# Kernel optimization log

Measured on AMD Instinct MI355X. Metric: run time of the kernel, lower is better.

## Reference

```python
import jax, jax.numpy as jnp
import numpy as np
import math

H, D = 8, 128            # num_heads, head_dim (hidden=1024)
CHUNK, PAST, FUT = 12, 12, 0
CTX = CHUNK + PAST + FUT  # 24
SOFTCAP = 50.0
INVALID = 1e-09
Q_SCALE = D ** (-0.5) / math.log(2)
K_SCALE = math.log(1.0 + math.e) / math.log(2)


def setup_inputs() -> dict:
    key = jax.random.key(0)
    ks = jax.random.split(key, 7)
    B, S, HS = 16, 2400, 1024
    w = lambda k: jax.random.normal(k, (HS, HS), jnp.float32) * 0.02
    return {
        "x": jax.random.normal(ks[0], (B, S, HS), jnp.float32),
        "pos_emb": jax.random.normal(ks[1], (CTX + 1, HS), jnp.float32),
        "Wq": w(ks[2]),
        "Wk": w(ks[3]),
        "Wv": w(ks[4]),
        "Wpost": w(ks[5]),
        "Wrel": w(ks[6]),
        "per_dim_scale": jnp.zeros((D,), jnp.float32),
    }


def _to_blocks(t):
    # [B,S,H,D] -> [B,nb,CHUNK,H,D] (pad S up to multiple of CHUNK)
    B, S, h, d = t.shape
    nb = -(-S // CHUNK)
    t = jnp.pad(t, ((0, 0), (0, nb * CHUNK - S), (0, 0), (0, 0)))
    return t.reshape(B, nb, CHUNK, h, d)


def _block_context(t):
    # [B,S,H,D] -> [B,nb,CTX,H,D]: per-block window of PAST left context + chunk + FUT
    B, S, h, d = t.shape
    nb = -(-S // CHUNK)
    tp = jnp.pad(t, ((0, 0), (PAST, FUT + CHUNK - 1), (0, 0), (0, 0)))
    idx = jnp.arange(nb)[:, None] * CHUNK + jnp.arange(CTX)[None, :]  # [nb,CTX]
    return tp[:, idx]  # gather -> [B,nb,CTX,H,D]


def _rel_shift(x):
    # [B,H,nb,CHUNK,P] -> [B,H,nb,CHUNK,CTX] via Transformer-XL reshape trick
    B, h, nb, bs, P = x.shape
    x = jnp.pad(x, ((0, 0), (0, 0), (0, 0), (0, 0), (0, CTX + 1 - P)))
    x = x.reshape(B, h, nb, bs * (CTX + 1))[..., : bs * CTX]
    return x.reshape(B, h, nb, bs, CTX)


def reference(x, pos_emb, Wq, Wk, Wv, Wpost, Wrel, per_dim_scale):
    B, S, HS = x.shape
    q = (x @ Wq).reshape(B, S, H, D) * Q_SCALE * jax.nn.softplus(per_dim_scale)
    k = (x @ Wk).reshape(B, S, H, D) * K_SCALE
    v = (x @ Wv).reshape(B, S, H, D)

    qb = _to_blocks(q)        # [B,nb,CHUNK,H,D]
    kc = _block_context(k)    # [B,nb,CTX,H,D]
    vc = _block_context(v)    # [B,nb,CTX,H,D]
    nb = qb.shape[1]

    rel_k = (pos_emb @ Wrel).reshape(-1, H, D)  # [P,H,D]

    # content-content scores: [B,H,nb,CHUNK,CTX]
    matrix_ac = jnp.einsum('bnqhd,bnkhd->bhnqk', qb, kc)
    # content-position scores with rel-shift: [B,H,nb,CHUNK,P] -> [...,CTX]
    matrix_bd = jnp.einsum('bnqhd,phd->bhnqp', qb, rel_k)
    matrix_bd = _rel_shift(matrix_bd)

    attn = jnp.tanh((matrix_ac + matrix_bd) / SOFTCAP) * SOFTCAP
    attn = jax.nn.softmax(attn, axis=-1)

    out = jnp.einsum('bhnqk,bnkhd->bnqhd', attn, vc)  # [B,nb,CHUNK,H,D]
    out = out.reshape(B, nb * CHUNK, H * D)[:, :S, :]
    return out @ Wpost
```

## Files before the change

### kernel.cpp

```cpp
#include <hip/hip_runtime.h>
#include <hip/hip_bf16.h>
#include <cmath>

#define AS_GLOBAL __attribute__((address_space(1)))
#define AS_LDS    __attribute__((address_space(3)))

typedef __attribute__((ext_vector_type(8))) short bf16x8;
typedef __attribute__((ext_vector_type(4))) float f32x4;
typedef unsigned short u16;

__device__ __forceinline__ u16 f2bf(float f) {
  union { __hip_bfloat16 h; u16 u; } cv;
  cv.h = __float2bfloat16(f);
  return cv.u;
}
__device__ __forceinline__ float bf2f(u16 u) {
  union { unsigned u32; float f; } v;
  v.u32 = ((unsigned)u) << 16;
  return v.f;
}


__global__ void k_f32_to_bf16(const float* __restrict__ in, u16* __restrict__ out, int n4) {
  int i = blockIdx.x * 256 + threadIdx.x;
  if (i >= n4) return;
  float4 v = ((const float4*)in)[i];
  ushort4 o;
  o.x = f2bf(v.x); o.y = f2bf(v.y); o.z = f2bf(v.z); o.w = f2bf(v.w);
  ((ushort4*)out)[i] = o;
}

__global__ void k_transpose_w(const float* __restrict__ in, u16* __restrict__ out) {
  __shared__ float tile[32][33];
  const int tx = threadIdx.x & 31;
  const int ty = threadIdx.x >> 5;
  const int x0 = blockIdx.x * 32, y0 = blockIdx.y * 32;
  #pragma unroll
  for (int i = 0; i < 32; i += 8)
    tile[ty + i][tx] = in[(size_t)(y0 + ty + i) * 1024 + x0 + tx];
  __syncthreads();
  #pragma unroll
  for (int i = 0; i < 32; i += 8)
    out[(size_t)(x0 + ty + i) * 1024 + y0 + tx] = f2bf(tile[tx][ty + i]);
}

__global__ void k_qscale(const float* __restrict__ pds, float* __restrict__ qs, float qscale_c) {
  int n = blockIdx.x * 256 + threadIdx.x;
  float s = pds[n & 127];
  qs[n] = qscale_c * log1pf(expf(s));
}

__global__ void k_relk(const float* __restrict__ pos, const u16* __restrict__ wrt,
                       u16* __restrict__ relkb) {
  __shared__ float prow[1024];
  const int tid = threadIdx.x;
  const int p = blockIdx.y;
  ((float4*)prow)[tid] = ((const float4*)(pos + (size_t)p * 1024))[tid];
  __syncthreads();
  int nn = blockIdx.x * 256 + tid;
  const u16* wr = wrt + (size_t)nn * 1024;
  float acc = 0.f;
  for (int kk = 0; kk < 1024; kk += 8) {
    ushort4 u0 = *(const ushort4*)(wr + kk);
    ushort4 u1 = *(const ushort4*)(wr + kk + 4);
    acc += bf2f(u0.x) * prow[kk + 0] + bf2f(u0.y) * prow[kk + 1]
         + bf2f(u0.z) * prow[kk + 2] + bf2f(u0.w) * prow[kk + 3]
         + bf2f(u1.x) * prow[kk + 4] + bf2f(u1.y) * prow[kk + 5]
         + bf2f(u1.z) * prow[kk + 6] + bf2f(u1.w) * prow[kk + 7];
  }
  relkb[(size_t)p * 1024 + nn] = f2bf(acc);
}

template <int OUTMODE>
__global__ __launch_bounds__(256) void k_gemm_bt(
    const u16* __restrict__ A, const u16* __restrict__ Bt, void* __restrict__ Cout,
    const float* __restrict__ scale_vec, float scale_scalar, int M, int N, int K) {
  __shared__ __align__(16) u16 As[128 * 32];
  __shared__ __align__(16) u16 Bs[128 * 32];
  const int tid = threadIdx.x;
  const int wave = tid >> 6, lane = tid & 63;
  const int quad = lane >> 4, l16 = lane & 15;
  const int wm = wave >> 1, wn = wave & 1;
  const int m0 = blockIdx.y * 128, n0 = blockIdx.x * 128;

  f32x4 acc[4][4];
  #pragma unroll
  for (int i = 0; i < 4; ++i)
    #pragma unroll
    for (int j = 0; j < 4; ++j) {
      f32x4 z = {0.f, 0.f, 0.f, 0.f};
      acc[i][j] = z;
    }

  for (int k0 = 0; k0 < K; k0 += 32) {
    __syncthreads();
    #pragma unroll
    for (int i = 0; i < 2; ++i) {
      int cbase = i * 256 + wave * 64;
      int c = cbase + lane;
      const u16* ga = A + (size_t)(m0 + (c >> 2)) * K + (k0 + (c & 3) * 8);
      __builtin_amdgcn_global_load_lds((const AS_GLOBAL u16*)ga, (AS_LDS u16*)&As[cbase * 8], 16, 0, 0);
      const u16* gb = Bt + (size_t)(n0 + (c >> 2)) * K + (k0 + (c & 3) * 8);
      __builtin_amdgcn_global_load_lds((const AS_GLOBAL u16*)gb, (AS_LDS u16*)&Bs[cbase * 8], 16, 0, 0);
    }
    __syncthreads();

    bf16x8 af[4], bfr[4];
    #pragma unroll
    for (int mi = 0; mi < 4; ++mi)
      af[mi] = *(const bf16x8*)&As[(wm * 64 + mi * 16 + l16) * 32 + quad * 8];
    #pragma unroll
    for (int ni = 0; ni < 4; ++ni)
      bfr[ni] = *(const bf16x8*)&Bs[(wn * 64 + ni * 16 + l16) * 32 + quad * 8];
    #pragma unroll
    for (int mi = 0; mi < 4; ++mi)
      #pragma unroll
      for (int ni = 0; ni < 4; ++ni)
        acc[mi][ni] = __builtin_amdgcn_mfma_f32_16x16x32_bf16(af[mi], bfr[ni], acc[mi][ni], 0, 0, 0);
  }

  if (OUTMODE == 2) {
    #pragma unroll
    for (int ni = 0; ni < 4; ++ni) {
      int col = n0 + wn * 64 + ni * 16 + l16;
      #pragma unroll
      for (int mi = 0; mi < 4; ++mi) {
        int row = m0 + wm * 64 + mi * 16 + quad * 4;
        ushort4 o;
        o.x = f2bf(acc[mi][ni][0]);
        o.y = f2bf(acc[mi][ni][1]);
        o.z = f2bf(acc[mi][ni][2]);
        o.w = f2bf(acc[mi][ni][3]);
        *(ushort4*)&((u16*)Cout)[(size_t)col * M + row] = o;
      }
    }
  } else {
    #pragma unroll
    for (int ni = 0; ni < 4; ++ni) {
      int col = n0 + wn * 64 + ni * 16 + l16;
      float cs = scale_vec ? scale_vec[col] : scale_scalar;
      #pragma unroll
      for (int mi = 0; mi < 4; ++mi) {
        int row = m0 + wm * 64 + mi * 16 + quad * 4;
        #pragma unroll
        for (int r = 0; r < 4; ++r) {
          float v = acc[mi][ni][r] * cs;
          if (OUTMODE == 1)
            ((u16*)Cout)[(size_t)(row + r) * N + col] = f2bf(v);
          else
            ((float*)Cout)[(size_t)(row + r) * N + col] = v;
        }
      }
    }
  }
}

__global__ __launch_bounds__(256) void k_attn_mfma(
    const u16* __restrict__ q, const u16* __restrict__ k, const u16* __restrict__ vt,
    const u16* __restrict__ relkb, u16* __restrict__ ctx) {
  __shared__ float bdm_s[4][400];
  __shared__ u16 attnb[4][16 * 32];

  const int tid = threadIdx.x;
  const int w = tid >> 6, lane = tid & 63;
  const int l16 = lane & 15, quad = lane >> 4;
  const int id = blockIdx.x * 4 + w;
  const int b = id / 1600;
  const int rr = id % 1600;
  const int n = rr >> 3, h = rr & 7;
  const int s0 = n * 12;
  const size_t rowbase = (size_t)b * 2400;

  bf16x8 qf[4];
  {
    int sq = s0 + l16;
    if (sq > 2399) sq = 2399;
    const u16* qp = q + ((rowbase + sq) * 1024 + (size_t)h * 128 + quad * 8);
    #pragma unroll
    for (int c = 0; c < 4; ++c) qf[c] = *(const bf16x8*)(qp + 32 * c);
  }

  #pragma unroll
  for (int pt = 0; pt < 2; ++pt) {
    int p = pt * 16 + l16;
    const u16* rp = relkb + ((size_t)p * 1024 + (size_t)h * 128 + quad * 8);
    f32x4 acc = {0.f, 0.f, 0.f, 0.f};
    #pragma unroll
    for (int c = 0; c < 4; ++c)
      acc = __builtin_amdgcn_mfma_f32_16x16x32_bf16(qf[c], *(const bf16x8*)(rp + 32 * c), acc, 0, 0, 0);
    if (p < 25) {
      #pragma unroll
      for (int r = 0; r < 4; ++r)
        bdm_s[w][(quad * 4 + r) * 25 + p] = acc[r];
    }
  }
  __threadfence_block();

  float l0[4], l1[4];
  #pragma unroll
  for (int kt = 0; kt < 2; ++kt) {
    int t = kt * 16 + l16;
    int sk = s0 - 12 + t;
    bool kvalid = ((unsigned)sk < 2400u);
    int ska = kvalid ? sk : 0;
    const u16* kp = k + ((rowbase + ska) * 1024 + (size_t)h * 128 + quad * 8);
    short km = kvalid ? (short)0xFFFF : (short)0;
    bf16x8 kmv = {km, km, km, km, km, km, km, km};
    f32x4 acc = {0.f, 0.f, 0.f, 0.f};
    #pragma unroll
    for (int c = 0; c < 4; ++c) {
      bf16x8 kf = *(const bf16x8*)(kp + 32 * c);
      kf &= kmv;
      acc = __builtin_amdgcn_mfma_f32_16x16x32_bf16(qf[c], kf, acc, 0, 0, 0);
    }
    #pragma unroll
    for (int r = 0; r < 4; ++r) {
      float bd = bdm_s[w][(quad * 4 + r) * 24 + t];
      float lg = tanhf((acc[r] + bd) * (1.0f / 50.0f)) * 50.0f;
      if (kt == 1 && l16 >= 8) lg = -INFINITY;
      if (kt) l1[r] = lg; else l0[r] = lg;
    }
  }

  float at0[4], at1[4];
  #pragma unroll
  for (int r = 0; r < 4; ++r) {
    float m = fmaxf(l0[r], l1[r]);
    #pragma unroll
    for (int s = 1; s < 16; s <<= 1) m = fmaxf(m, __shfl_xor(m, s, 64));
    float e0 = __expf(l0[r] - m), e1 = __expf(l1[r] - m);
    float sum = e0 + e1;
    #pragma unroll
    for (int s = 1; s < 16; s <<= 1) sum += __shfl_xor(sum, s, 64);
    float inv = 1.0f / sum;
    at0[r] = e0 * inv;
    at1[r] = e1 * inv;
  }

  #pragma unroll
  for (int r = 0; r < 4; ++r) {
    attnb[w][(quad * 4 + r) * 32 + l16] = f2bf(at0[r]);
    attnb[w][(quad * 4 + r) * 32 + 16 + l16] = f2bf(at1[r]);
  }
  __threadfence_block();
  bf16x8 af = *(const bf16x8*)&attnb[w][l16 * 32 + quad * 8];

  int slo = s0 - 12 + quad * 8;
  bf16x8 vmsk;
  #pragma unroll
  for (int j = 0; j < 8; ++j)
    vmsk[j] = ((unsigned)(slo + j) < 2400u) ? (short)0xFFFF : (short)0;

  f32x4 oacc[8];
  #pragma unroll
  for (int dt = 0; dt < 8; ++dt) {
    int col = h * 128 + dt * 16 + l16;
    const u16* vp = vt + ((size_t)col * 38400 + (long)(rowbase + s0 - 12 + quad * 8));
    ushort4 va = *(const ushort4*)vp;
    ushort4 vb = *(const ushort4*)(vp + 4);
    bf16x8 vf = {(short)va.x, (short)va.y, (short)va.z, (short)va.w,
                 (short)vb.x, (short)vb.y, (short)vb.z, (short)vb.w};
    vf &= vmsk;
    f32x4 z = {0.f, 0.f, 0.f, 0.f};
    oacc[dt] = __builtin_amdgcn_mfma_f32_16x16x32_bf16(af, vf, z, 0, 0, 0);
  }

  if (quad < 3) {
    #pragma unroll
    for (int dt = 0; dt < 8; ++dt) {
      int col = h * 128 + dt * 16 + l16;
      #pragma unroll
      for (int r = 0; r < 4; ++r) {
        int qi = quad * 4 + r;
        ctx[(rowbase + s0 + qi) * 1024 + col] = f2bf(oacc[dt][r]);
      }
    }
  }
}


extern "C" void kernel_launch(void* const* d_in, const int* in_sizes, int n_in,
                              void* d_out, int out_size, void* d_ws, size_t ws_size,
                              hipStream_t stream) {
  const float* x       = (const float*)d_in[0];
  const float* pos_emb = (const float*)d_in[1];
  const float* Wq      = (const float*)d_in[2];
  const float* Wk      = (const float*)d_in[3];
  const float* Wv      = (const float*)d_in[4];
  const float* Wpost   = (const float*)d_in[5];
  const float* Wrel    = (const float*)d_in[6];
  const float* pds     = (const float*)d_in[7];
  float* out = (float*)d_out;

  const int M = 38400, HS = 1024;
  const size_t XE = (size_t)M * HS;

  u16* xbf = (u16*)d_ws;
  u16* qbf = xbf + XE;
  u16* kbf = qbf + XE;
  u16* vt_alloc = kbf + XE;
  u16* vt = vt_alloc + 16;
  u16* wqt = vt_alloc + XE + 64;
  u16* wkt = wqt + (size_t)HS * HS;
  u16* wvt = wkt + (size_t)HS * HS;
  u16* wrt = wvt + (size_t)HS * HS;
  u16* wpt = wrt + (size_t)HS * HS;
  u16* relkb = wpt + (size_t)HS * HS;
  float* qsc = (float*)(relkb + 32 * 1024);

  const double LN2 = 0.6931471805599453;
  const float QS = (float)((1.0 / sqrt(128.0)) / LN2);
  const float KS = (float)(log(1.0 + exp(1.0)) / LN2);

  k_f32_to_bf16<<<(int)(XE / 4 / 256), 256, 0, stream>>>(x, xbf, (int)(XE / 4));
  dim3 tg(32, 32);
  k_transpose_w<<<tg, 256, 0, stream>>>(Wq, wqt);
  k_transpose_w<<<tg, 256, 0, stream>>>(Wk, wkt);
  k_transpose_w<<<tg, 256, 0, stream>>>(Wv, wvt);
  k_transpose_w<<<tg, 256, 0, stream>>>(Wrel, wrt);
  k_transpose_w<<<tg, 256, 0, stream>>>(Wpost, wpt);
  k_qscale<<<4, 256, 0, stream>>>(pds, qsc, QS);
  k_relk<<<dim3(4, 25), 256, 0, stream>>>(pos_emb, wrt, relkb);
  dim3 gg(HS / 128, M / 128);
  k_gemm_bt<1><<<gg, 256, 0, stream>>>(xbf, wqt, qbf, qsc, 1.0f, M, HS, HS);
  k_gemm_bt<1><<<gg, 256, 0, stream>>>(xbf, wkt, kbf, nullptr, KS, M, HS, HS);
  k_gemm_bt<2><<<gg, 256, 0, stream>>>(xbf, wvt, vt, nullptr, 1.0f, M, HS, HS);
  k_attn_mfma<<<25600 / 4, 256, 0, stream>>>(qbf, kbf, vt, relkb, xbf);
  k_gemm_bt<0><<<gg, 256, 0, stream>>>(xbf, wpt, out, nullptr, 1.0f, M, HS, HS);
}
```

Before: 950.4 us.

## Replace GEMMs with pipelined 256x256 tile kernel, fuse QKV, persistent attention

Replaces the simple 128x128 GEMM with a 256x256-tile, 512-thread kernel. The new kernel double-buffers LDS through direct global-to-LDS loads, uses swizzled LDS addressing, interleaves MFMA with fine-grained waitcnt/barrier staging, and applies a grid-swizzled tile order. The Q, K and V projections become one launch over a concatenated N=3072 weight, with section-specific epilogues. The attention kernel becomes a grid-stride loop over 2048 blocks. The intent is higher MFMA utilisation and fewer launches, at the cost of relying on wqt/wkt/wvt being contiguous and on K being a multiple of 128.

```diff
diff --git a/kernel.cpp b/kernel.cpp
--- a/kernel.cpp
+++ b/kernel.cpp
@@ -71,89 +71,203 @@
   relkb[(size_t)p * 1024 + nn] = f2bf(acc);
 }
 
-template <int OUTMODE>
-__global__ __launch_bounds__(256) void k_gemm_bt(
-    const u16* __restrict__ A, const u16* __restrict__ Bt, void* __restrict__ Cout,
-    const float* __restrict__ scale_vec, float scale_scalar, int M, int N, int K) {
-  __shared__ __align__(16) u16 As[128 * 32];
-  __shared__ __align__(16) u16 Bs[128 * 32];
-  const int tid = threadIdx.x;
-  const int wave = tid >> 6, lane = tid & 63;
-  const int quad = lane >> 4, l16 = lane & 15;
-  const int wm = wave >> 1, wn = wave & 1;
-  const int m0 = blockIdx.y * 128, n0 = blockIdx.x * 128;
-
-  f32x4 acc[4][4];
+
+#define VMCNT(n) do { asm volatile("s_waitcnt vmcnt(" #n ")" ::: "memory"); \
+                      __builtin_amdgcn_sched_barrier(0); } while (0)
+#define BARF() do { asm volatile("" ::: "memory"); __builtin_amdgcn_s_barrier(); asm volatile("" ::: "memory"); } while (0)
+#define GLD(SRC, DST) __builtin_amdgcn_global_load_lds((const AS_GLOBAL u16*)(SRC), (AS_LDS u16*)(DST), 16, 0, 0)
+#define LDSA(d) ((AS_LDS char*)&lds[d][0][0])
+#define LDSB(d) ((AS_LDS char*)&lds[d][1][0])
+
+#define STAGE_A(d, h, t) do {                                                   \
+  GLD(sA0 + (((size_t)(h)) << 6) * K + ((t) << 6), LDSA(d) + dA0 + ((h) << 13)); \
+  GLD(sA1 + (((size_t)(h)) << 6) * K + ((t) << 6), LDSA(d) + dA1 + ((h) << 13)); \
+} while (0)
+#define STAGE_B(d, h, t) do {                                                   \
+  GLD(sB0 + (((size_t)(h)) << 5) * K + ((t) << 6), LDSB(d) + dB0 + ((h) << 12)); \
+  GLD(sB1 + (((size_t)(h)) << 5) * K + ((t) << 6), LDSB(d) + dB1 + ((h) << 12)); \
+} while (0)
+
+#define LOAD_A(d, qm) do {                                                       \
+  _Pragma("unroll") for (int mi_ = 0; mi_ < 4; ++mi_) {                          \
+    af[mi_][0] = *(const bf16x8*)&lds[d][0][abase + (((qm)*64 + mi_*16) << 6) + gk0]; \
+    af[mi_][1] = *(const bf16x8*)&lds[d][0][abase + (((qm)*64 + mi_*16) << 6) + gk1]; \
+  } } while (0)
+#define LOAD_B(d, qn) do {                                                       \
+  _Pragma("unroll") for (int ni_ = 0; ni_ < 2; ++ni_) {                          \
+    bfb[ni_][0] = *(const bf16x8*)&lds[d][1][bbase + (((qn)*32 + ni_*16) << 6) + gk0]; \
+    bfb[ni_][1] = *(const bf16x8*)&lds[d][1][bbase + (((qn)*32 + ni_*16) << 6) + gk1]; \
+  } } while (0)
+#define MFMA16(qm, qn) do {                                                      \
+  __builtin_amdgcn_s_setprio(1);                                                 \
+  _Pragma("unroll") for (int mi_ = 0; mi_ < 4; ++mi_)                            \
+  _Pragma("unroll") for (int ni_ = 0; ni_ < 2; ++ni_) {                          \
+    acc[(qm)*4+mi_][(qn)*2+ni_] = __builtin_amdgcn_mfma_f32_16x16x32_bf16(       \
+        af[mi_][0], bfb[ni_][0], acc[(qm)*4+mi_][(qn)*2+ni_], 0, 0, 0);          \
+    acc[(qm)*4+mi_][(qn)*2+ni_] = __builtin_amdgcn_mfma_f32_16x16x32_bf16(       \
+        af[mi_][1], bfb[ni_][1], acc[(qm)*4+mi_][(qn)*2+ni_], 0, 0, 0);          \
+  }                                                                              \
+  __builtin_amdgcn_s_setprio(0); } while (0)
+
+#define GEMM_MAINLOOP()                                                          \
+  STAGE_B(0, 0, 0);  STAGE_A(0, 1, 0);  STAGE_A(0, 0, 0);  STAGE_B(0, 1, 0);     \
+  STAGE_B(1, 0, 1);  STAGE_A(1, 1, 1);                                           \
+  VMCNT(6);  BARF();                                                             \
+  const int nk = K >> 6;                                                         \
+  for (int i = 0; i < (nk >> 1) - 1; ++i) {                                      \
+    const int t1 = 2 * i + 1, t2 = 2 * i + 2, t3 = 2 * i + 3;                    \
+    LOAD_A(0, 0); LOAD_B(0, 0);                                                  \
+    STAGE_A(1, 0, t1);                                                           \
+    BARF(); MFMA16(0, 0); BARF();                                                \
+    LOAD_A(0, 1);                                                                \
+    STAGE_B(1, 1, t1);                                                           \
+    BARF(); MFMA16(1, 0); VMCNT(8); BARF();                                      \
+    LOAD_B(0, 1);                                                                \
+    STAGE_B(0, 0, t2);                                                           \
+    BARF(); MFMA16(1, 1); BARF();                                                \
+    LOAD_A(0, 0);                                                                \
+    STAGE_A(0, 1, t2);                                                           \
+    BARF(); MFMA16(0, 1); VMCNT(6); BARF();                                      \
+    LOAD_A(1, 0); LOAD_B(1, 0);                                                  \
+    STAGE_A(0, 0, t2);                                                           \
+    BARF(); MFMA16(0, 0); BARF();                                                \
+    LOAD_A(1, 1);                                                                \
+    STAGE_B(0, 1, t2);                                                           \
+    BARF(); MFMA16(1, 0); VMCNT(8); BARF();                                      \
+    LOAD_B(1, 1);                                                                \
+    STAGE_B(1, 0, t3);                                                           \
+    BARF(); MFMA16(1, 1); BARF();                                                \
+    LOAD_A(1, 0);                                                                \
+    STAGE_A(1, 1, t3);                                                           \
+    BARF(); MFMA16(0, 1); VMCNT(6); BARF();                                      \
+  }                                                                              \
+  {                                                                              \
+    const int t1 = nk - 1;                                                       \
+    LOAD_A(0, 0); LOAD_B(0, 0);                                                  \
+    STAGE_A(1, 0, t1);                                                           \
+    BARF(); MFMA16(0, 0); BARF();                                                \
+    LOAD_A(0, 1);                                                                \
+    STAGE_B(1, 1, t1);                                                           \
+    BARF(); MFMA16(1, 0); VMCNT(8); BARF();                                      \
+    LOAD_B(0, 1);                                                                \
+    BARF(); MFMA16(1, 1); BARF();                                                \
+    LOAD_A(0, 0);                                                                \
+    BARF(); MFMA16(0, 1); VMCNT(2); BARF();                                      \
+    LOAD_A(1, 0); LOAD_B(1, 0);                                                  \
+    BARF(); MFMA16(0, 0); BARF();                                                \
+    LOAD_A(1, 1);                                                                \
+    BARF(); MFMA16(1, 0); VMCNT(0); BARF();                                      \
+    LOAD_B(1, 1);                                                                \
+    BARF(); MFMA16(1, 1); BARF();                                                \
+    LOAD_A(1, 0);                                                                \
+    BARF(); MFMA16(0, 1);                                                        \
+  }
+
+#define GEMM_SETUP(NTN)                                                          \
+  __shared__ __align__(16) u16 lds[2][2][16384];                                 \
+  const int tid = threadIdx.x;                                                   \
+  const int wave = tid >> 6, lane = tid & 63;                                    \
+  const int l16 = lane & 15, quad = lane >> 4;                                   \
+  const int wm = wave >> 2, wn = wave & 3;                                       \
+  const int q8 = (int)gridDim.x >> 3;                                            \
+  const int wg = ((int)blockIdx.x & 7) * q8 + ((int)blockIdx.x >> 3);            \
+  const int m0 = (wg / (NTN)) << 8;                                              \
+  const int n0 = (wg % (NTN)) << 8;                                              \
+  const int sx = l16 & 7;                                                        \
+  const int gk0 = (quad ^ sx) << 3;                                              \
+  const int gk1 = ((4 + quad) ^ sx) << 3;                                        \
+  const int abase = (wm * 128 + l16) << 6;                                       \
+  const int bbase = (wn * 64 + l16) << 6;                                        \
+  const int rl0 = tid >> 3, g0 = tid & 7;                                        \
+  const int rl1 = rl0 + 64;                                                      \
+  const int swz0 = (g0 ^ (rl0 & 7)) << 3;                                        \
+  const int rbA0 = ((rl0 >> 6) << 7) + (rl0 & 63);                               \
+  const int rbA1 = ((rl1 >> 6) << 7) + (rl1 & 63);                               \
+  const int rbB0 = ((rl0 >> 5) << 6) + (rl0 & 31);                               \
+  const int rbB1 = ((rl1 >> 5) << 6) + (rl1 & 31);                               \
+  const u16* sA0 = A + (size_t)(m0 + rbA0) * K + swz0;                           \
+  const u16* sA1 = A + (size_t)(m0 + rbA1) * K + swz0;                           \
+  const u16* sB0 = Bt + (size_t)(n0 + rbB0) * K + swz0;                          \
+  const u16* sB1 = Bt + (size_t)(n0 + rbB1) * K + swz0;                          \
+  const int dA0 = (rbA0 << 7) + (g0 << 4);                                       \
+  const int dA1 = (rbA1 << 7) + (g0 << 4);                                       \
+  const int dB0 = (rbB0 << 7) + (g0 << 4);                                       \
+  const int dB1 = (rbB1 << 7) + (g0 << 4);                                       \
+  f32x4 acc[8][4];                                                               \
+  _Pragma("unroll") for (int i = 0; i < 8; ++i)                                  \
+    _Pragma("unroll") for (int j = 0; j < 4; ++j) {                              \
+      f32x4 z = {0.f, 0.f, 0.f, 0.f};                                            \
+      acc[i][j] = z;                                                             \
+    }                                                                            \
+  bf16x8 af[4][2], bfb[2][2];
+
+__global__ __launch_bounds__(512, 2) void k_gemm256(
+    const u16* __restrict__ A, const u16* __restrict__ Bt, float* __restrict__ Cout,
+    int M, int N, int K) {
+  GEMM_SETUP(N >> 8)
+  GEMM_MAINLOOP()
+  const int mb = m0 + wm * 128, nb = n0 + wn * 64;
   #pragma unroll
-  for (int i = 0; i < 4; ++i)
-    #pragma unroll
-    for (int j = 0; j < 4; ++j) {
-      f32x4 z = {0.f, 0.f, 0.f, 0.f};
-      acc[i][j] = z;
-    }
-
-  for (int k0 = 0; k0 < K; k0 += 32) {
-    __syncthreads();
-    #pragma unroll
-    for (int i = 0; i < 2; ++i) {
-      int cbase = i * 256 + wave * 64;
-      int c = cbase + lane;
-      const u16* ga = A + (size_t)(m0 + (c >> 2)) * K + (k0 + (c & 3) * 8);
-      __builtin_amdgcn_global_load_lds((const AS_GLOBAL u16*)ga, (AS_LDS u16*)&As[cbase * 8], 16, 0, 0);
-      const u16* gb = Bt + (size_t)(n0 + (c >> 2)) * K + (k0 + (c & 3) * 8);
-      __builtin_amdgcn_global_load_lds((const AS_GLOBAL u16*)gb, (AS_LDS u16*)&Bs[cbase * 8], 16, 0, 0);
-    }
-    __syncthreads();
-
-    bf16x8 af[4], bfr[4];
-    #pragma unroll
-    for (int mi = 0; mi < 4; ++mi)
-      af[mi] = *(const bf16x8*)&As[(wm * 64 + mi * 16 + l16) * 32 + quad * 8];
-    #pragma unroll
-    for (int ni = 0; ni < 4; ++ni)
-      bfr[ni] = *(const bf16x8*)&Bs[(wn * 64 + ni * 16 + l16) * 32 + quad * 8];
-    #pragma unroll
-    for (int mi = 0; mi < 4; ++mi)
-      #pragma unroll
-      for (int ni = 0; ni < 4; ++ni)
-        acc[mi][ni] = __builtin_amdgcn_mfma_f32_16x16x32_bf16(af[mi], bfr[ni], acc[mi][ni], 0, 0, 0);
+  for (int ni = 0; ni < 4; ++ni) {
+    int col = nb + ni * 16 + l16;
+    #pragma unroll
+    for (int mi = 0; mi < 8; ++mi) {
+      int row = mb + mi * 16 + quad * 4;
+      #pragma unroll
+      for (int r = 0; r < 4; ++r)
+        Cout[(size_t)(row + r) * N + col] = acc[mi][ni][r];
+    }
   }
-
-  if (OUTMODE == 2) {
+}
+
+__global__ __launch_bounds__(512, 2) void k_gemm_qkv(
+    const u16* __restrict__ A, const u16* __restrict__ Bt,
+    u16* __restrict__ Qo, u16* __restrict__ Ko, u16* __restrict__ Vt,
+    const float* __restrict__ qsc, float ks, int M, int K) {
+  GEMM_SETUP(12)
+  GEMM_MAINLOOP()
+  const int sec = n0 >> 10;
+  const int mb = m0 + wm * 128;
+  const int nbl = (n0 & 1023) + wn * 64;
+  if (sec == 2) {
     #pragma unroll
     for (int ni = 0; ni < 4; ++ni) {
-      int col = n0 + wn * 64 + ni * 16 + l16;
-      #pragma unroll
-      for (int mi = 0; mi < 4; ++mi) {
-        int row = m0 + wm * 64 + mi * 16 + quad * 4;
+      int col = nbl + ni * 16 + l16;
+      #pragma unroll
+      for (int mi = 0; mi < 8; ++mi) {
+        int row = mb + mi * 16 + quad * 4;
         ushort4 o;
         o.x = f2bf(acc[mi][ni][0]);
         o.y = f2bf(acc[mi][ni][1]);
         o.z = f2bf(acc[mi][ni][2]);
         o.w = f2bf(acc[mi][ni][3]);
-        *(ushort4*)&((u16*)Cout)[(size_t)col * M + row] = o;
+        *(ushort4*)&Vt[(size_t)col * M + row] = o;
       }
     }
   } else {
+    u16* Out = (sec == 0) ? Qo : Ko;
     #pragma unroll
     for (int ni = 0; ni < 4; ++ni) {
-      int col = n0 + wn * 64 + ni * 16 + l16;
-      float cs = scale_vec ? scale_vec[col] : scale_scalar;
-      #pragma unroll
-      for (int mi = 0; mi < 4; ++mi) {
-        int row = m0 + wm * 64 + mi * 16 + quad * 4;
+      int col = nbl + ni * 16 + l16;
+      float cs = (sec == 0) ? qsc[col] : ks;
+      #pragma unroll
+      for (int mi = 0; mi < 8; ++mi) {
+        int row = mb + mi * 16 + quad * 4;
         #pragma unroll
-        for (int r = 0; r < 4; ++r) {
-          float v = acc[mi][ni][r] * cs;
-          if (OUTMODE == 1)
-            ((u16*)Cout)[(size_t)(row + r) * N + col] = f2bf(v);
-          else
-            ((float*)Cout)[(size_t)(row + r) * N + col] = v;
-        }
+        for (int r = 0; r < 4; ++r)
+          Out[(size_t)(row + r) * 1024 + col] = f2bf(acc[mi][ni][r] * cs);
       }
     }
   }
 }
+
+#undef GEMM_SETUP
+#undef GEMM_MAINLOOP
+#undef STAGE_A
+#undef STAGE_B
+#undef LOAD_A
+#undef LOAD_B
+#undef MFMA16
 
 __global__ __launch_bounds__(256) void k_attn_mfma(
     const u16* __restrict__ q, const u16* __restrict__ k, const u16* __restrict__ vt,
@@ -164,115 +278,118 @@
   const int tid = threadIdx.x;
   const int w = tid >> 6, lane = tid & 63;
   const int l16 = lane & 15, quad = lane >> 4;
-  const int id = blockIdx.x * 4 + w;
-  const int b = id / 1600;
-  const int rr = id % 1600;
-  const int n = rr >> 3, h = rr & 7;
-  const int s0 = n * 12;
-  const size_t rowbase = (size_t)b * 2400;
-
-  bf16x8 qf[4];
-  {
-    int sq = s0 + l16;
-    if (sq > 2399) sq = 2399;
-    const u16* qp = q + ((rowbase + sq) * 1024 + (size_t)h * 128 + quad * 8);
-    #pragma unroll
-    for (int c = 0; c < 4; ++c) qf[c] = *(const bf16x8*)(qp + 32 * c);
-  }
-
-  #pragma unroll
-  for (int pt = 0; pt < 2; ++pt) {
-    int p = pt * 16 + l16;
-    const u16* rp = relkb + ((size_t)p * 1024 + (size_t)h * 128 + quad * 8);
-    f32x4 acc = {0.f, 0.f, 0.f, 0.f};
-    #pragma unroll
-    for (int c = 0; c < 4; ++c)
-      acc = __builtin_amdgcn_mfma_f32_16x16x32_bf16(qf[c], *(const bf16x8*)(rp + 32 * c), acc, 0, 0, 0);
-    if (p < 25) {
-      #pragma unroll
-      for (int r = 0; r < 4; ++r)
-        bdm_s[w][(quad * 4 + r) * 25 + p] = acc[r];
-    }
-  }
-  __threadfence_block();
-
-  float l0[4], l1[4];
-  #pragma unroll
-  for (int kt = 0; kt < 2; ++kt) {
-    int t = kt * 16 + l16;
-    int sk = s0 - 12 + t;
-    bool kvalid = ((unsigned)sk < 2400u);
-    int ska = kvalid ? sk : 0;
-    const u16* kp = k + ((rowbase + ska) * 1024 + (size_t)h * 128 + quad * 8);
-    short km = kvalid ? (short)0xFFFF : (short)0;
-    bf16x8 kmv = {km, km, km, km, km, km, km, km};
-    f32x4 acc = {0.f, 0.f, 0.f, 0.f};
-    #pragma unroll
-    for (int c = 0; c < 4; ++c) {
-      bf16x8 kf = *(const bf16x8*)(kp + 32 * c);
-      kf &= kmv;
-      acc = __builtin_amdgcn_mfma_f32_16x16x32_bf16(qf[c], kf, acc, 0, 0, 0);
-    }
+
+  for (int id0 = (int)blockIdx.x * 4; id0 < 25600; id0 += (int)gridDim.x * 4) {
+    const int id = id0 + w;
+    const int b = id / 1600;
+    const int rr = id % 1600;
+    const int n = rr >> 3, h = rr & 7;
+    const int s0 = n * 12;
+    const size_t rowbase = (size_t)b * 2400;
+
+    bf16x8 qf[4];
+    {
+      int sq = s0 + l16;
+      if (sq > 2399) sq = 2399;
+      const u16* qp = q + ((rowbase + sq) * 1024 + (size_t)h * 128 + quad * 8);
+      #pragma unroll
+      for (int c = 0; c < 4; ++c) qf[c] = *(const bf16x8*)(qp + 32 * c);
+    }
+
+    #pragma unroll
+    for (int pt = 0; pt < 2; ++pt) {
+      int p = pt * 16 + l16;
+      const u16* rp = relkb + ((size_t)p * 1024 + (size_t)h * 128 + quad * 8);
+      f32x4 acc = {0.f, 0.f, 0.f, 0.f};
+      #pragma unroll
+      for (int c = 0; c < 4; ++c)
+        acc = __builtin_amdgcn_mfma_f32_16x16x32_bf16(qf[c], *(const bf16x8*)(rp + 32 * c), acc, 0, 0, 0);
+      if (p < 25) {
+        #pragma unroll
+        for (int r = 0; r < 4; ++r)
+          bdm_s[w][(quad * 4 + r) * 25 + p] = acc[r];
+      }
+    }
+    __threadfence_block();
+
+    float l0[4], l1[4];
+    #pragma unroll
+    for (int kt = 0; kt < 2; ++kt) {
+      int t = kt * 16 + l16;
+      int sk = s0 - 12 + t;
+      bool kvalid = ((unsigned)sk < 2400u);
+      int ska = kvalid ? sk : 0;
+      const u16* kp = k + ((rowbase + ska) * 1024 + (size_t)h * 128 + quad * 8);
+      short km = kvalid ? (short)0xFFFF : (short)0;
+      bf16x8 kmv = {km, km, km, km, km, km, km, km};
+      f32x4 acc = {0.f, 0.f, 0.f, 0.f};
+      #pragma unroll
+      for (int c = 0; c < 4; ++c) {
+        bf16x8 kf = *(const bf16x8*)(kp + 32 * c);
+        kf &= kmv;
+        acc = __builtin_amdgcn_mfma_f32_16x16x32_bf16(qf[c], kf, acc, 0, 0, 0);
+      }
+      #pragma unroll
+      for (int r = 0; r < 4; ++r) {
+        float bd = bdm_s[w][(quad * 4 + r) * 24 + t];
+        float lg = tanhf((acc[r] + bd) * (1.0f / 50.0f)) * 50.0f;
+        if (kt == 1 && l16 >= 8) lg = -INFINITY;
+        if (kt) l1[r] = lg; else l0[r] = lg;
+      }
+    }
+
+    float at0[4], at1[4];
     #pragma unroll
     for (int r = 0; r < 4; ++r) {
-      float bd = bdm_s[w][(quad * 4 + r) * 24 + t];
-      float lg = tanhf((acc[r] + bd) * (1.0f / 50.0f)) * 50.0f;
-      if (kt == 1 && l16 >= 8) lg = -INFINITY;
-      if (kt) l1[r] = lg; else l0[r] = lg;
-    }
-  }
-
-  float at0[4], at1[4];
-  #pragma unroll
-  for (int r = 0; r < 4; ++r) {
-    float m = fmaxf(l0[r], l1[r]);
-    #pragma unroll
-    for (int s = 1; s < 16; s <<= 1) m = fmaxf(m, __shfl_xor(m, s, 64));
-    float e0 = __expf(l0[r] - m), e1 = __expf(l1[r] - m);
-    float sum = e0 + e1;
-    #pragma unroll
-    for (int s = 1; s < 16; s <<= 1) sum += __shfl_xor(sum, s, 64);
-    float inv = 1.0f / sum;
-    at0[r] = e0 * inv;
-    at1[r] = e1 * inv;
-  }
-
-  #pragma unroll
-  for (int r = 0; r < 4; ++r) {
-    attnb[w][(quad * 4 + r) * 32 + l16] = f2bf(at0[r]);
-    attnb[w][(quad * 4 + r) * 32 + 16 + l16] = f2bf(at1[r]);
-  }
-  __threadfence_block();
-  bf16x8 af = *(const bf16x8*)&attnb[w][l16 * 32 + quad * 8];
-
-  int slo = s0 - 12 + quad * 8;
-  bf16x8 vmsk;
-  #pragma unroll
-  for (int j = 0; j < 8; ++j)
-    vmsk[j] = ((unsigned)(slo + j) < 2400u) ? (short)0xFFFF : (short)0;
-
-  f32x4 oacc[8];
-  #pragma unroll
-  for (int dt = 0; dt < 8; ++dt) {
-    int col = h * 128 + dt * 16 + l16;
-    const u16* vp = vt + ((size_t)col * 38400 + (long)(rowbase + s0 - 12 + quad * 8));
-    ushort4 va = *(const ushort4*)vp;
-    ushort4 vb = *(const ushort4*)(vp + 4);
-    bf16x8 vf = {(short)va.x, (short)va.y, (short)va.z, (short)va.w,
-                 (short)vb.x, (short)vb.y, (short)vb.z, (short)vb.w};
-    vf &= vmsk;
-    f32x4 z = {0.f, 0.f, 0.f, 0.f};
-    oacc[dt] = __builtin_amdgcn_mfma_f32_16x16x32_bf16(af, vf, z, 0, 0, 0);
-  }
-
-  if (quad < 3) {
+      float m = fmaxf(l0[r], l1[r]);
+      #pragma unroll
+      for (int s = 1; s < 16; s <<= 1) m = fmaxf(m, __shfl_xor(m, s, 64));
+      float e0 = __expf(l0[r] - m), e1 = __expf(l1[r] - m);
+      float sum = e0 + e1;
+      #pragma unroll
+      for (int s = 1; s < 16; s <<= 1) sum += __shfl_xor(sum, s, 64);
+      float inv = 1.0f / sum;
+      at0[r] = e0 * inv;
+      at1[r] = e1 * inv;
+    }
+
+    #pragma unroll
+    for (int r = 0; r < 4; ++r) {
+      attnb[w][(quad * 4 + r) * 32 + l16] = f2bf(at0[r]);
+      attnb[w][(quad * 4 + r) * 32 + 16 + l16] = f2bf(at1[r]);
+    }
+    __threadfence_block();
+    bf16x8 paf = *(const bf16x8*)&attnb[w][l16 * 32 + quad * 8];
+
+    int slo = s0 - 12 + quad * 8;
+    bf16x8 vmsk;
+    #pragma unroll
+    for (int j = 0; j < 8; ++j)
+      vmsk[j] = ((unsigned)(slo + j) < 2400u) ? (short)0xFFFF : (short)0;
+
+    f32x4 oacc[8];
     #pragma unroll
     for (int dt = 0; dt < 8; ++dt) {
       int col = h * 128 + dt * 16 + l16;
-      #pragma unroll
-      for (int r = 0; r < 4; ++r) {
-        int qi = quad * 4 + r;
-        ctx[(rowbase + s0 + qi) * 1024 + col] = f2bf(oacc[dt][r]);
+      const u16* vp = vt + ((size_t)col * 38400 + (long)(rowbase + s0 - 12 + quad * 8));
+      ushort4 va = *(const ushort4*)vp;
+      ushort4 vb = *(const ushort4*)(vp + 4);
+      bf16x8 vf = {(short)va.x, (short)va.y, (short)va.z, (short)va.w,
+                   (short)vb.x, (short)vb.y, (short)vb.z, (short)vb.w};
+      vf &= vmsk;
+      f32x4 z = {0.f, 0.f, 0.f, 0.f};
+      oacc[dt] = __builtin_amdgcn_mfma_f32_16x16x32_bf16(paf, vf, z, 0, 0, 0);
+    }
+
+    if (quad < 3) {
+      #pragma unroll
+      for (int dt = 0; dt < 8; ++dt) {
+        int col = h * 128 + dt * 16 + l16;
+        #pragma unroll
+        for (int r = 0; r < 4; ++r) {
+          int qi = quad * 4 + r;
+          ctx[(rowbase + s0 + qi) * 1024 + col] = f2bf(oacc[dt][r]);
+        }
       }
     }
   }
@@ -321,10 +438,7 @@
   k_transpose_w<<<tg, 256, 0, stream>>>(Wpost, wpt);
   k_qscale<<<4, 256, 0, stream>>>(pds, qsc, QS);
   k_relk<<<dim3(4, 25), 256, 0, stream>>>(pos_emb, wrt, relkb);
-  dim3 gg(HS / 128, M / 128);
-  k_gemm_bt<1><<<gg, 256, 0, stream>>>(xbf, wqt, qbf, qsc, 1.0f, M, HS, HS);
-  k_gemm_bt<1><<<gg, 256, 0, stream>>>(xbf, wkt, kbf, nullptr, KS, M, HS, HS);
-  k_gemm_bt<2><<<gg, 256, 0, stream>>>(xbf, wvt, vt, nullptr, 1.0f, M, HS, HS);
-  k_attn_mfma<<<25600 / 4, 256, 0, stream>>>(qbf, kbf, vt, relkb, xbf);
-  k_gemm_bt<0><<<gg, 256, 0, stream>>>(xbf, wpt, out, nullptr, 1.0f, M, HS, HS);
-}
+  k_gemm_qkv<<<(M / 256) * 12, 512, 0, stream>>>(xbf, wqt, qbf, kbf, vt, qsc, KS, M, HS);
+  k_attn_mfma<<<2048, 256, 0, stream>>>(qbf, kbf, vt, relkb, xbf);
+  k_gemm256<<<(M / 256) * (HS / 256), 512, 0, stream>>>(xbf, wpt, out, M, HS, HS);
+}
```

Measured after the change: 798.3 us. 1.19x faster.
